# Kernel tuning notes

Hardware: AMD Instinct MI355X
Metric: run time of the kernel (lower is better)

The kernel has to match this reference:

```python
import jax, jax.numpy as jnp
import numpy as np

N_BINS = 15


def setup_inputs() -> dict:
    key = jax.random.key(0)
    k1, k2 = jax.random.split(key)
    N, C = 131072, 1000
    labels = jax.random.randint(k1, (N,), 0, C, dtype=jnp.int64)
    logits = jax.random.normal(k2, (N, C), dtype=jnp.float32)
    return {"labels": labels, "logits": logits}


def reference(labels, logits):
    # softmax then (confidence, prediction) = max over classes
    probs = jax.nn.softmax(logits, axis=-1)            # [N, C]
    confidences = jnp.max(probs, axis=1)               # [N]
    predictions = jnp.argmax(probs, axis=1)            # [N]
    accuracies = (predictions == labels).astype(jnp.float32)

    bounds = jnp.linspace(0.0, 1.0, N_BINS + 1)
    lowers, uppers = bounds[:-1], bounds[1:]
    # bins are (lower, upper], matching gt/le in the torch code
    in_bin = (confidences[None, :] > lowers[:, None]) & (
        confidences[None, :] <= uppers[:, None]
    )                                                   # [n_bins, N]
    mask = in_bin.astype(jnp.float32)
    counts = mask.sum(axis=1)                           # [n_bins]
    n = jnp.float32(confidences.shape[0])
    prop_in_bin = counts / n
    sum_conf = mask @ confidences                       # [n_bins]
    sum_acc = mask @ accuracies                         # [n_bins]
    safe = jnp.maximum(counts, 1.0)
    gap = jnp.abs(sum_conf / safe - sum_acc / safe)
    ece = jnp.sum(jnp.where(counts > 0, gap * prop_in_bin, 0.0))
    return (100.0 * ece).reshape(1)  # percent=True
```

## Files before the change

kernel.cpp:

```cpp
#include <hip/hip_runtime.h>
#include <math.h>

#define NBINS 15
#define NGRP  (NBINS * 3)

__device__ __forceinline__ float exp2_fast(float x) {
#if __has_builtin(__builtin_amdgcn_exp2f)
    return __builtin_amdgcn_exp2f(x);
#else
    return exp2f(x);
#endif
}

template<int NCHUNK_CT>
__global__ __launch_bounds__(256) void ece_phase1(
        const float* __restrict__ logits,
        const int*   __restrict__ labels,
        float*       __restrict__ ws,
        int N, int C, int NB) {
    __shared__ float s_cnt[NBINS];
    __shared__ float s_conf[NBINS];
    __shared__ float s_acc[NBINS];

    const int tid = threadIdx.x;
    if (tid < NBINS) { s_cnt[tid] = 0.0f; s_conf[tid] = 0.0f; s_acc[tid] = 0.0f; }
    __syncthreads();

    const int lane   = tid & 63;
    const int wib    = tid >> 6;
    const int wpb    = blockDim.x >> 6;
    const int waveId = blockIdx.x * wpb + wib;
    const int nWaves = gridDim.x * wpb;
    const int nchunk = NCHUNK_CT ? NCHUNK_CT : (C >> 2);
    const float L2E  = 1.4426950408889634f;

    int vl[4];
    #pragma unroll
    for (int j = 0; j < 4; ++j) {
        int v = nchunk - 64 * j;
        vl[j] = v < 0 ? 0 : (v > 64 ? 64 : v);
    }

    auto loadrow = [&](float4* v, int r, int& lab) {
        const float4* rp = (const float4*)(logits + (size_t)r * (size_t)C);
        #pragma unroll
        for (int j = 0; j < 4; ++j) {
            int q = lane + 64 * j;
            q = (q < nchunk) ? q : (nchunk - 1);
            v[j] = rp[q];
        }
        lab = labels[r];
    };

    auto compute = [&](const float4* v, int lab) {
        float pmax = -INFINITY;
        float psum = 0.0f;
        #pragma unroll
        for (int j = 0; j < 4; ++j) {
            float ej = exp2_fast(v[j].x * L2E) + exp2_fast(v[j].y * L2E)
                     + exp2_fast(v[j].z * L2E) + exp2_fast(v[j].w * L2E);
            if (NCHUNK_CT ? (vl[j] < 64) : true)
                ej = (lane < vl[j]) ? ej : 0.0f;
            psum += ej;
            pmax = fmaxf(pmax,
                   fmaxf(fmaxf(v[j].x, v[j].y), fmaxf(v[j].z, v[j].w)));
        }

        #pragma unroll
        for (int msk = 32; msk; msk >>= 1) {
            float om = __shfl_xor(pmax, msk, 64);
            float os = __shfl_xor(psum, msk, 64);
            pmax = fmaxf(pmax, om);
            psum += os;
        }
        const float m = pmax;
        const float S = psum;

        bool pred = false;
        #pragma unroll
        for (int j = 0; j < 4; ++j) {
            const int e0 = (lane + 64 * j) << 2;
            const int d  = lab - e0;
            if ((unsigned)d < 4u) {
                float val = (d == 0) ? v[j].x : (d == 1) ? v[j].y
                          : (d == 2) ? v[j].z : v[j].w;
                pred = (val == m);
            }
        }
        const bool hit = (__ballot(pred) != 0ull);

        if (lane == 0) {
            const float conf = exp2_fast(m * L2E) / S;
            int b = NBINS - 1;
            #pragma unroll
            for (int i = 0; i < NBINS; ++i) {
                float ub = (float)((double)(i + 1) / (double)NBINS);
                if (conf <= ub) { b = i; break; }
            }
            atomicAdd(&s_cnt[b],  1.0f);
            atomicAdd(&s_conf[b], conf);
            atomicAdd(&s_acc[b],  hit ? 1.0f : 0.0f);
        }
    };

    float4 A[4], B[4], Cb[4];
    int labA = 0, labB = 0, labC = 0;

    int  ra = waveId, rb = ra + nWaves;
    bool hA = (ra < N), hB = (rb < N);
    if (hA) loadrow(A, ra, labA);
    if (hB) loadrow(B, rb, labB);

    while (hA) {
        const int  rc = rb + nWaves; const bool hC = (rc < N);
        if (hC) loadrow(Cb, rc, labC);
        compute(A, labA);
        if (!hB) break;

        const int  rd = rc + nWaves; const bool hD = (rd < N);
        if (hD) loadrow(A, rd, labA);
        compute(B, labB);
        if (!hC) break;

        const int  re = rd + nWaves; const bool hE = (re < N);
        if (hE) loadrow(B, re, labB);
        compute(Cb, labC);
        if (!hD) break;

        ra = rd; rb = re; hA = hD; hB = hE;
    }

    __syncthreads();
    if (tid < NGRP) {
        const int stat = tid / NBINS;
        const int bin  = tid % NBINS;
        const float v  = (stat == 0) ? s_cnt[bin]
                       : (stat == 1) ? s_conf[bin] : s_acc[bin];
        ws[(size_t)tid * (size_t)NB + (size_t)blockIdx.x] = v;
    }
}

__global__ __launch_bounds__(256) void ece_phase2(
        const float* __restrict__ ws, float* __restrict__ sums, int NB) {
    __shared__ float s_w[4];
    const int g    = blockIdx.x;
    const int tid  = threadIdx.x;
    const int lane = tid & 63;
    const int wib  = tid >> 6;

    const float* p = ws + (size_t)g * (size_t)NB;
    float s = 0.0f;
    for (int i = tid; i < NB; i += 256) s += p[i];
    #pragma unroll
    for (int msk = 32; msk; msk >>= 1) s += __shfl_xor(s, msk, 64);
    if (lane == 0) s_w[wib] = s;
    __syncthreads();
    if (tid == 0) sums[g] = s_w[0] + s_w[1] + s_w[2] + s_w[3];
}

__global__ void ece_phase3(const float* __restrict__ sums,
                           float* __restrict__ out, int N) {
    if (threadIdx.x == 0 && blockIdx.x == 0) {
        float ece = 0.0f;
        for (int i = 0; i < NBINS; ++i) {
            float cnt = sums[i];
            float sc  = sums[NBINS + i];
            float sa  = sums[2 * NBINS + i];
            float safe = fmaxf(cnt, 1.0f);
            float gap  = fabsf(sc / safe - sa / safe);
            if (cnt > 0.0f) ece += gap * (cnt / (float)N);
        }
        out[0] = 100.0f * ece;
    }
}

extern "C" void kernel_launch(void* const* d_in, const int* in_sizes, int n_in,
                              void* d_out, int out_size, void* d_ws, size_t ws_size,
                              hipStream_t stream) {
    const int*   labels = (const int*)d_in[0];
    const float* logits = (const float*)d_in[1];
    float*       out    = (float*)d_out;
    float*       ws     = (float*)d_ws;

    const int N = in_sizes[0];
    const int C = in_sizes[1] / in_sizes[0];

    int NB = 2048;
    while (NB > 64 && (size_t)(NGRP * NB + NGRP) * sizeof(float) > ws_size)
        NB >>= 1;
    float* sums = ws + (size_t)NGRP * (size_t)NB;

    if (C == 1000)
        ece_phase1<250><<<NB, 256, 0, stream>>>(logits, labels, ws, N, C, NB);
    else
        ece_phase1<0><<<NB, 256, 0, stream>>>(logits, labels, ws, N, C, NB);

    ece_phase2<<<NGRP, 256, 0, stream>>>(ws, sums, NB);
    ece_phase3<<<1, 64, 0, stream>>>(sums, out, N);
}
```

Before: 104.5 us.

## Cut register pressure in ECE row kernel: double buffer, precomputed offsets, fused label check

The specialised C=1000 kernel drops from triple to double buffering of rows and asks for 8 blocks per CU through launch bounds, aiming for higher occupancy. Load offsets are precomputed as byte offsets, so only the last chunk needs a clamp. The label-value lookup is folded into the exp/max loop so the row registers can be freed sooner. A separate simple generic kernel now handles other C values. Keeping fewer rows in flight per wave relies on the extra occupancy to hide memory latency, and it may not.

```diff
diff --git a/kernel.cpp b/kernel.cpp
--- a/kernel.cpp
+++ b/kernel.cpp
@@ -13,7 +13,7 @@
 }
 
 template<int NCHUNK_CT>
-__global__ __launch_bounds__(256) void ece_phase1(
+__global__ __launch_bounds__(256, 8) void ece_phase1(
         const float* __restrict__ logits,
         const int*   __restrict__ labels,
         float*       __restrict__ ws,
@@ -27,45 +27,45 @@
     __syncthreads();
 
     const int lane   = tid & 63;
-    const int wib    = tid >> 6;
+    const int wib    = __builtin_amdgcn_readfirstlane(tid >> 6);
     const int wpb    = blockDim.x >> 6;
     const int waveId = blockIdx.x * wpb + wib;
     const int nWaves = gridDim.x * wpb;
     const int nchunk = NCHUNK_CT ? NCHUNK_CT : (C >> 2);
     const float L2E  = 1.4426950408889634f;
 
-    int vl[4];
-    #pragma unroll
-    for (int j = 0; j < 4; ++j) {
-        int v = nchunk - 64 * j;
-        vl[j] = v < 0 ? 0 : (v > 64 ? 64 : v);
-    }
+    const int off0 = lane << 4;
+    const int t3   = nchunk - 192;
+    const int off3 = ((lane < t3) ? (lane + 192) : (nchunk - 1)) << 4;
 
     auto loadrow = [&](float4* v, int r, int& lab) {
-        const float4* rp = (const float4*)(logits + (size_t)r * (size_t)C);
-        #pragma unroll
-        for (int j = 0; j < 4; ++j) {
-            int q = lane + 64 * j;
-            q = (q < nchunk) ? q : (nchunk - 1);
-            v[j] = rp[q];
-        }
-        lab = labels[r];
+        const char* base = (const char*)logits + (size_t)r * (size_t)C * 4u;
+        v[0] = *(const float4*)(base + off0);
+        v[1] = *(const float4*)(base + off0 + 1024);
+        v[2] = *(const float4*)(base + off0 + 2048);
+        v[3] = *(const float4*)(base + off3);
+        lab  = labels[r];
     };
 
     auto compute = [&](const float4* v, int lab) {
-        float pmax = -INFINITY;
-        float psum = 0.0f;
+        float pmax = -INFINITY, psum = 0.0f, labval = 0.0f;
+        bool  own  = false;
         #pragma unroll
         for (int j = 0; j < 4; ++j) {
             float ej = exp2_fast(v[j].x * L2E) + exp2_fast(v[j].y * L2E)
                      + exp2_fast(v[j].z * L2E) + exp2_fast(v[j].w * L2E);
-            if (NCHUNK_CT ? (vl[j] < 64) : true)
-                ej = (lane < vl[j]) ? ej : 0.0f;
+            if (j == 3) ej = (lane < t3) ? ej : 0.0f;
             psum += ej;
             pmax = fmaxf(pmax,
                    fmaxf(fmaxf(v[j].x, v[j].y), fmaxf(v[j].z, v[j].w)));
-        }
-
+            const int e0 = (lane + 64 * j) << 2;
+            const int d  = lab - e0;
+            if ((unsigned)d < 4u) {
+                labval = (d == 0) ? v[j].x : (d == 1) ? v[j].y
+                       : (d == 2) ? v[j].z : v[j].w;
+                own = true;
+            }
+        }
         #pragma unroll
         for (int msk = 32; msk; msk >>= 1) {
             float om = __shfl_xor(pmax, msk, 64);
@@ -73,24 +73,10 @@
             pmax = fmaxf(pmax, om);
             psum += os;
         }
-        const float m = pmax;
-        const float S = psum;
-
-        bool pred = false;
-        #pragma unroll
-        for (int j = 0; j < 4; ++j) {
-            const int e0 = (lane + 64 * j) << 2;
-            const int d  = lab - e0;
-            if ((unsigned)d < 4u) {
-                float val = (d == 0) ? v[j].x : (d == 1) ? v[j].y
-                          : (d == 2) ? v[j].z : v[j].w;
-                pred = (val == m);
-            }
-        }
-        const bool hit = (__ballot(pred) != 0ull);
+        const bool hit = (__ballot(own && (labval == pmax)) != 0ull);
 
         if (lane == 0) {
-            const float conf = exp2_fast(m * L2E) / S;
+            const float conf = exp2_fast(pmax * L2E) / psum;
             int b = NBINS - 1;
             #pragma unroll
             for (int i = 0; i < NBINS; ++i) {
@@ -103,31 +89,85 @@
         }
     };
 
-    float4 A[4], B[4], Cb[4];
-    int labA = 0, labB = 0, labC = 0;
-
-    int  ra = waveId, rb = ra + nWaves;
-    bool hA = (ra < N), hB = (rb < N);
-    if (hA) loadrow(A, ra, labA);
-    if (hB) loadrow(B, rb, labB);
-
+    float4 A[4], B[4];
+    int labA = 0, labB = 0;
+
+    int  rowA = waveId;
+    bool hA   = (rowA < N);
+    if (hA) loadrow(A, rowA, labA);
     while (hA) {
-        const int  rc = rb + nWaves; const bool hC = (rc < N);
-        if (hC) loadrow(Cb, rc, labC);
+        const int  rowB = rowA + nWaves;
+        const bool hB   = (rowB < N);
+        if (hB) loadrow(B, rowB, labB);
         compute(A, labA);
         if (!hB) break;
-
-        const int  rd = rc + nWaves; const bool hD = (rd < N);
-        if (hD) loadrow(A, rd, labA);
+        rowA = rowB + nWaves;
+        hA   = (rowA < N);
+        if (hA) loadrow(A, rowA, labA);
         compute(B, labB);
-        if (!hC) break;
-
-        const int  re = rd + nWaves; const bool hE = (re < N);
-        if (hE) loadrow(B, re, labB);
-        compute(Cb, labC);
-        if (!hD) break;
-
-        ra = rd; rb = re; hA = hD; hB = hE;
+    }
+
+    __syncthreads();
+    if (tid < NGRP) {
+        const int stat = tid / NBINS;
+        const int bin  = tid % NBINS;
+        const float v  = (stat == 0) ? s_cnt[bin]
+                       : (stat == 1) ? s_conf[bin] : s_acc[bin];
+        ws[(size_t)tid * (size_t)NB + (size_t)blockIdx.x] = v;
+    }
+}
+
+__global__ __launch_bounds__(256) void ece_phase1_generic(
+        const float* __restrict__ logits,
+        const int*   __restrict__ labels,
+        float*       __restrict__ ws,
+        int N, int C, int NB) {
+    __shared__ float s_cnt[NBINS];
+    __shared__ float s_conf[NBINS];
+    __shared__ float s_acc[NBINS];
+
+    const int tid = threadIdx.x;
+    if (tid < NBINS) { s_cnt[tid] = 0.0f; s_conf[tid] = 0.0f; s_acc[tid] = 0.0f; }
+    __syncthreads();
+
+    const int lane   = tid & 63;
+    const int wib    = tid >> 6;
+    const int wpb    = blockDim.x >> 6;
+    const int waveId = blockIdx.x * wpb + wib;
+    const int nWaves = gridDim.x * wpb;
+    const float L2E  = 1.4426950408889634f;
+
+    for (int row = waveId; row < N; row += nWaves) {
+        const float* rp = logits + (size_t)row * (size_t)C;
+        const int lab = labels[row];
+        float pmax = -INFINITY, psum = 0.0f, labval = 0.0f;
+        bool own = false;
+        for (int e = lane; e < C; e += 64) {
+            float x = rp[e];
+            pmax = fmaxf(pmax, x);
+            psum += exp2_fast(x * L2E);
+            if (e == lab) { labval = x; own = true; }
+        }
+        #pragma unroll
+        for (int msk = 32; msk; msk >>= 1) {
+            float om = __shfl_xor(pmax, msk, 64);
+            float os = __shfl_xor(psum, msk, 64);
+            pmax = fmaxf(pmax, om);
+            psum += os;
+        }
+        const bool hit = (__ballot(own && (labval == pmax)) != 0ull);
+        if (lane == 0) {
+            const float conf = exp2_fast(pmax * L2E) / psum;
+            int b = NBINS - 1;
+            #pragma unroll
+            for (int i = 0; i < NBINS; ++i) {
+                float ub = (float)((double)(i + 1) / (double)NBINS);
+                if (conf <= ub) { b = i; break; }
+            }
+            atomicAdd(&s_cnt[b],  1.0f);
+            atomicAdd(&s_conf[b], conf);
+            atomicAdd(&s_acc[b],  hit ? 1.0f : 0.0f);
+        }
     }
 
     __syncthreads();
@@ -193,7 +233,7 @@
     if (C == 1000)
         ece_phase1<250><<<NB, 256, 0, stream>>>(logits, labels, ws, N, C, NB);
     else
-        ece_phase1<0><<<NB, 256, 0, stream>>>(logits, labels, ws, N, C, NB);
+        ece_phase1_generic<<<NB, 256, 0, stream>>>(logits, labels, ws, N, C, NB);
 
     ece_phase2<<<NGRP, 256, 0, stream>>>(ws, sums, NB);
     ece_phase3<<<1, 64, 0, stream>>>(sums, out, N);
```

Result: no change. 104.0 us (-0.5%).
